# Performance work log

Hardware: AMD Instinct MI355X
Metric: run time of the kernel (lower is better)

Reference implementation:

```python
import math
import jax, jax.numpy as jnp
import numpy as np

B, S, H, NH = 2, 1536, 2048, 16
DH = H // NH  # 128
FP16_MIN = float(jnp.finfo(jnp.float16).min)


def setup_inputs() -> dict:
    key = jax.random.key(0)
    ks = jax.random.split(key, 6)
    std = 0.02
    return {
        "x": jax.random.normal(ks[0], (B, S, H), dtype=jnp.float32),
        "attention_bias": jax.random.normal(ks[1], (B, NH, S, S), dtype=jnp.float32),
        "Wq": jax.random.normal(ks[2], (H, H), dtype=jnp.float32) * std,
        "Wk": jax.random.normal(ks[3], (H, H), dtype=jnp.float32) * std,
        "Wv": jax.random.normal(ks[4], (H, H), dtype=jnp.float32) * std,
        "Wo": jax.random.normal(ks[5], (H, H), dtype=jnp.float32) * std,
    }


def reference(x, attention_bias, Wq, Wk, Wv, Wo):
    b, s, h = x.shape
    # QKV projections (nn.Linear with bias=False: y = x @ W.T)
    q = (x @ Wq.T).reshape(b, s, NH, DH).transpose(0, 2, 1, 3)  # b h s d
    k = (x @ Wk.T).reshape(b, s, NH, DH).transpose(0, 2, 1, 3)
    v = (x @ Wv.T).reshape(b, s, NH, DH).transpose(0, 2, 1, 3)
    # bias[:, :, -s:, -s:] is identity here since bias is already [b,h,s,s]
    bias = attention_bias[:, :, -s:, -s:]
    # mask where tril(bias) == 0 (upper triangle and any exact zeros in lower)
    masked = jnp.tril(bias) == 0
    bias = jnp.where(masked, FP16_MIN, bias)
    # torch SDPA default scale = 1/sqrt(head_dim) (module's softmax_scale unused)
    scale = 1.0 / math.sqrt(DH)
    scores = jnp.einsum("bhqd,bhkd->bhqk", q, k) * scale + bias
    attn = jax.nn.softmax(scores, axis=-1)
    out = jnp.einsum("bhqk,bhkd->bhqd", attn, v)  # b h s d
    out = out.transpose(0, 2, 1, 3).reshape(b, s, h)  # b s (h d)
    return out @ Wo.T
```

## Files before the change

### kernel.cpp

```cpp
#include <hip/hip_runtime.h>
#include <cstdint>
#include <stddef.h>

typedef short short8 __attribute__((ext_vector_type(8)));
typedef float floatx4 __attribute__((ext_vector_type(4)));
typedef unsigned short ushortx4 __attribute__((ext_vector_type(4)));

#define MFMA16(a, b, c) __builtin_amdgcn_mfma_f32_16x16x32_bf16((a), (b), (c), 0, 0, 0)

static constexpr int Bv = 2, Sv = 1536, Hv = 2048, NHv = 16, DHv = 128;
static constexpr int Mv = Bv * Sv;
static constexpr float SCALE = 0.08838834764831845f;

__device__ inline unsigned short f2bf(float f) {
  union { float f; unsigned u; } c; c.f = f;
  unsigned u = c.u;
  u += 0x7fffu + ((u >> 16) & 1u);
  return (unsigned short)(u >> 16);
}

__device__ inline void async_copy16(const void* g, void* l) {
  auto gp = reinterpret_cast<__attribute__((address_space(1))) uint32_t*>(
      reinterpret_cast<uintptr_t>(g));
  auto lp = reinterpret_cast<__attribute__((address_space(3))) uint32_t*>(
      reinterpret_cast<uintptr_t>(l));
  __builtin_amdgcn_global_load_lds(gp, lp, 16, 0, 0);
}

__global__ void cvt_all_kernel(const float* __restrict__ x,
    const float* __restrict__ Wq, const float* __restrict__ Wk,
    const float* __restrict__ Wv, const float* __restrict__ Wo,
    unsigned short* __restrict__ xb, unsigned short* __restrict__ wqb,
    unsigned short* __restrict__ wkb, unsigned short* __restrict__ wvb,
    unsigned short* __restrict__ wob) {
  const int i = blockIdx.x * 256 + threadIdx.x;
  const int nx4 = (Mv * Hv) / 4;
  const float* src; unsigned short* dst; int j; float scl = 1.0f;
  if (i < nx4) {
    src = x; dst = xb; j = i;
  } else {
    const int i2 = i - nx4;
    const int wsel = i2 >> 20;
    j = i2 & ((1 << 20) - 1);
    if (wsel == 0)      { src = Wq; dst = wqb; scl = SCALE; }
    else if (wsel == 1) { src = Wk; dst = wkb; }
    else if (wsel == 2) { src = Wv; dst = wvb; }
    else                { src = Wo; dst = wob; }
  }
  const float4 v = reinterpret_cast<const float4*>(src)[j];
  ushortx4 o;
  o[0] = f2bf(v.x * scl); o[1] = f2bf(v.y * scl);
  o[2] = f2bf(v.z * scl); o[3] = f2bf(v.w * scl);
  reinterpret_cast<ushortx4*>(dst)[j] = o;
}

template <int TM, bool WF32>
__global__ __launch_bounds__(256) void gemm_bt_kernel(
    const unsigned short* __restrict__ A,
    const unsigned short* __restrict__ W0, const unsigned short* __restrict__ W1,
    const unsigned short* __restrict__ W2,
    void* __restrict__ C0, void* __restrict__ C1, void* __restrict__ C2) {
  constexpr int MI = TM / 32;
  __shared__ __align__(16) unsigned short As[TM * 64];
  __shared__ __align__(16) unsigned short Bs[128 * 64];
  const int z = blockIdx.z;
  const unsigned short* W = (z == 0) ? W0 : ((z == 1) ? W1 : W2);
  const int tid = threadIdx.x;
  const int w = tid >> 6, lane = tid & 63;
  const int quad = lane >> 4, l15 = lane & 15;
  const int wr = w >> 1, wc = w & 1;
  const int tileM = blockIdx.y * TM, tileN = blockIdx.x * 128;

  floatx4 acc[MI][4];
#pragma unroll
  for (int i = 0; i < MI; ++i)
#pragma unroll
    for (int j = 0; j < 4; ++j)
#pragma unroll
      for (int r = 0; r < 4; ++r) acc[i][j][r] = 0.0f;

  size_t aoff[MI]; int alb[MI];
#pragma unroll
  for (int m = 0; m < MI; ++m) {
    const int slot = m * 256 + tid;
    const int row = slot >> 3, blk = slot & 7;
    aoff[m] = (size_t)(tileM + row) * 2048 + ((blk ^ (row & 7)) * 8);
    alb[m] = (m * 256 + w * 64) * 8;
  }
  size_t boff[4]; int blb[4];
#pragma unroll
  for (int m = 0; m < 4; ++m) {
    const int slot = m * 256 + tid;
    const int row = slot >> 3, blk = slot & 7;
    boff[m] = (size_t)(tileN + row) * 2048 + ((blk ^ (row & 7)) * 8);
    blb[m] = (m * 256 + w * 64) * 8;
  }

  for (int k0 = 0; k0 < 2048; k0 += 64) {
    __syncthreads();
#pragma unroll
    for (int m = 0; m < MI; ++m) async_copy16(A + aoff[m] + k0, As + alb[m]);
#pragma unroll
    for (int m = 0; m < 4; ++m) async_copy16(W + boff[m] + k0, Bs + blb[m]);
    __syncthreads();
#pragma unroll
    for (int kk = 0; kk < 2; ++kk) {
      const int swz = (((kk * 4 + quad) ^ (l15 & 7)) * 8);
      short8 af[MI], bfr[4];
#pragma unroll
      for (int i = 0; i < MI; ++i)
        af[i] = *(const short8*)(As + (wr * (TM / 2) + i * 16 + l15) * 64 + swz);
#pragma unroll
      for (int j = 0; j < 4; ++j)
        bfr[j] = *(const short8*)(Bs + (wc * 64 + j * 16 + l15) * 64 + swz);
#pragma unroll
      for (int i = 0; i < MI; ++i)
#pragma unroll
        for (int j = 0; j < 4; ++j) acc[i][j] = MFMA16(af[i], bfr[j], acc[i][j]);
    }
  }

  void* C = (z == 0) ? C0 : ((z == 1) ? C1 : C2);
#pragma unroll
  for (int i = 0; i < MI; ++i) {
#pragma unroll
    for (int r = 0; r < 4; ++r) {
      const int row = tileM + wr * (TM / 2) + i * 16 + quad * 4 + r;
#pragma unroll
      for (int j = 0; j < 4; ++j) {
        const int col = tileN + wc * 64 + j * 16 + l15;
        if (WF32)
          ((float*)C)[(size_t)row * 2048 + col] = acc[i][j][r];
        else
          ((unsigned short*)C)[(size_t)row * 2048 + col] = f2bf(acc[i][j][r]);
      }
    }
  }
}

__global__ __launch_bounds__(256) void vtrans_kernel(
    const unsigned short* __restrict__ V, unsigned short* __restrict__ Vtg) {
  __shared__ unsigned short Vs[64 * 132];
  const int t0 = blockIdx.x * 64, h = blockIdx.y, b = blockIdx.z;
  const int tid = threadIdx.x;
  const int w = tid >> 6, lane = tid & 63;
#pragma unroll
  for (int m = 0; m < 4; ++m) {
    const int idx = m * 256 + tid;
    const int tr = idx >> 4, blk = idx & 15;
    const unsigned short* src = V + ((size_t)(b * Sv) + t0 + tr) * Hv + h * DHv + blk * 8;
    ushortx4 v0 = *(const ushortx4*)(src);
    ushortx4 v1 = *(const ushortx4*)(src + 4);
    *(ushortx4*)(Vs + tr * 132 + blk * 8) = v0;
    *(ushortx4*)(Vs + tr * 132 + blk * 8 + 4) = v1;
  }
  __syncthreads();
  const size_t obase = ((size_t)(b * NHv + h) * DHv) * Sv + t0;
#pragma unroll 4
  for (int p = 0; p < 32; ++p) {
    const int d = p * 4 + w;
    Vtg[obase + (size_t)d * Sv + lane] = Vs[lane * 132 + d];
  }
}

__global__ __launch_bounds__(256) void attn_kernel(
    const unsigned short* __restrict__ Qg, const unsigned short* __restrict__ Kg,
    const unsigned short* __restrict__ Vtg, const float* __restrict__ bias,
    unsigned short* __restrict__ Og) {
  __shared__ __align__(16) unsigned short Ks[64 * 128];
  __shared__ __align__(16) unsigned short Vt[128 * 64];
  __shared__ __align__(16) unsigned short Ps[4 * 16 * 64];

  const int xb = blockIdx.x;
  const int qt = (xb & 1) ? (23 - (xb >> 1)) : (xb >> 1);
  const int h = blockIdx.y, b = blockIdx.z;
  const int q0 = qt * 64;
  const int tid = threadIdx.x;
  const int w = tid >> 6, lane = tid & 63;
  const int quad = lane >> 4, l15 = lane & 15;

  const size_t bh_base = (size_t)(b * Sv) * Hv + (size_t)h * DHv;
  const size_t vt_base = ((size_t)(b * NHv + h) * DHv) * Sv;

  short8 qf[4];
  {
    const unsigned short* qbase = Qg + bh_base + (size_t)(q0 + w * 16 + l15) * Hv;
#pragma unroll
    for (int kk = 0; kk < 4; ++kk)
      qf[kk] = *(const short8*)(qbase + kk * 32 + quad * 8);
  }

  floatx4 o[8];
#pragma unroll
  for (int n = 0; n < 8; ++n)
#pragma unroll
    for (int r = 0; r < 4; ++r) o[n][r] = 0.0f;
  float lrow[4] = {0.0f, 0.0f, 0.0f, 0.0f};

  const float* biasbase = bias + (size_t)(b * NHv + h) * Sv * Sv;
  unsigned short* pw = Ps + w * 1024;

  size_t koff[4], voff[4]; int lbs[4];
#pragma unroll
  for (int m = 0; m < 4; ++m) {
    const int sK = m * 256 + tid;
    const int rK = sK >> 4, bK = sK & 15;
    koff[m] = bh_base + (size_t)rK * Hv + ((bK ^ (rK & 15)) * 8);
    const int sV = m * 256 + tid;
    const int rV = sV >> 3, bV = sV & 7;
    voff[m] = vt_base + (size_t)rV * Sv + ((bV ^ (rV & 7)) * 8);
    lbs[m] = (m * 256 + w * 64) * 8;
  }

  float bv[4][4];
#pragma unroll
  for (int r = 0; r < 4; ++r) {
    const size_t brow = (size_t)(q0 + w * 16 + quad * 4 + r) * Sv;
#pragma unroll
    for (int j = 0; j < 4; ++j) bv[r][j] = biasbase[brow + j * 16 + l15];
  }

  for (int kt = 0; kt <= qt; ++kt) {
    const int k0 = kt * 64;
    __syncthreads();
#pragma unroll
    for (int m = 0; m < 4; ++m) {
      async_copy16(Kg + koff[m] + (size_t)k0 * Hv, Ks + lbs[m]);
      async_copy16(Vtg + voff[m] + k0, Vt + lbs[m]);
    }
    __syncthreads();

    const int kn = (kt < qt) ? k0 + 64 : k0;
    float bvn[4][4];
#pragma unroll
    for (int r = 0; r < 4; ++r) {
      const size_t brow = (size_t)(q0 + w * 16 + quad * 4 + r) * Sv;
#pragma unroll
      for (int j = 0; j < 4; ++j) bvn[r][j] = biasbase[brow + kn + j * 16 + l15];
    }

    floatx4 sacc[4];
#pragma unroll
    for (int j = 0; j < 4; ++j) {
#pragma unroll
      for (int r = 0; r < 4; ++r) sacc[j][r] = 0.0f;
      const int kr = j * 16 + l15;
#pragma unroll
      for (int kk = 0; kk < 4; ++kk) {
        const int g = kk * 4 + quad;
        short8 bfrag = *(const short8*)(Ks + kr * 128 + (g ^ (kr & 15)) * 8);
        sacc[j] = MFMA16(qf[kk], bfrag, sacc[j]);
      }
    }

    const bool diag = (kt == qt);
#pragma unroll
    for (int r = 0; r < 4; ++r) {
      const int qrow = q0 + w * 16 + quad * 4 + r;
      const int prow = quad * 4 + r;
      float acc_l = 0.0f;
#pragma unroll
      for (int j = 0; j < 4; ++j) {
        const int col = j * 16 + l15;
        float p = __expf(sacc[j][r] + bv[r][j]);
        if (diag && (k0 + col) > qrow) p = 0.0f;
        acc_l += p;
        pw[prow * 64 + ((col >> 3) ^ (prow & 7)) * 8 + (col & 7)] = f2bf(p);
      }
      lrow[r] += acc_l;
    }
#pragma unroll
    for (int r = 0; r < 4; ++r)
#pragma unroll
      for (int j = 0; j < 4; ++j) bv[r][j] = bvn[r][j];

#pragma unroll
    for (int kk = 0; kk < 2; ++kk) {
      const int g = kk * 4 + quad;
      short8 pa = *(const short8*)(pw + l15 * 64 + (g ^ (l15 & 7)) * 8);
#pragma unroll
      for (int n = 0; n < 8; ++n) {
        const int dr = n * 16 + l15;
        short8 vbf = *(const short8*)(Vt + dr * 64 + (g ^ (dr & 7)) * 8);
        o[n] = MFMA16(pa, vbf, o[n]);
      }
    }
  }

#pragma unroll
  for (int r = 0; r < 4; ++r) {
    float ls = lrow[r];
#pragma unroll
    for (int off = 1; off < 16; off <<= 1) ls += __shfl_xor(ls, off, 64);
    const float inv = 1.0f / ls;
    const int qrow = q0 + w * 16 + quad * 4 + r;
    const size_t rowbase = bh_base + (size_t)qrow * Hv;
#pragma unroll
    for (int n = 0; n < 8; ++n)
      Og[rowbase + n * 16 + l15] = f2bf(o[n][r] * inv);
  }
}

extern "C" void kernel_launch(void* const* d_in, const int* in_sizes, int n_in,
                              void* d_out, int out_size, void* d_ws, size_t ws_size,
                              hipStream_t stream) {
  const float* x = (const float*)d_in[0];
  const float* bias = (const float*)d_in[1];
  const float* Wq = (const float*)d_in[2];
  const float* Wk = (const float*)d_in[3];
  const float* Wv = (const float*)d_in[4];
  const float* Wo = (const float*)d_in[5];
  float* out = (float*)d_out;

  unsigned short* xb = (unsigned short*)d_ws;
  unsigned short* wqb = xb + (size_t)Mv * Hv;
  unsigned short* wkb = wqb + (size_t)Hv * Hv;
  unsigned short* wvb = wkb + (size_t)Hv * Hv;
  unsigned short* wob = wvb + (size_t)Hv * Hv;
  unsigned short* qb = wob + (size_t)Hv * Hv;
  unsigned short* kb = qb + (size_t)Mv * Hv;
  unsigned short* vb = kb + (size_t)Mv * Hv;
  unsigned short* ob = vb + (size_t)Mv * Hv;
  unsigned short* vtb = xb;
  const size_t needed = ((size_t)Mv * Hv * 5 + (size_t)Hv * Hv * 4) * 2;
  if (ws_size < needed) return;

  const int cvt_n = (Mv * Hv) / 4 + Hv * Hv;
  cvt_all_kernel<<<dim3(cvt_n / 256), 256, 0, stream>>>(
      x, Wq, Wk, Wv, Wo, xb, wqb, wkb, wvb, wob);

  gemm_bt_kernel<128, false><<<dim3(16, 24, 3), 256, 0, stream>>>(
      xb, wqb, wkb, wvb, qb, kb, vb);

  vtrans_kernel<<<dim3(24, 16, 2), 256, 0, stream>>>(vb, vtb);

  attn_kernel<<<dim3(24, NHv, Bv), 256, 0, stream>>>(qb, kb, vtb, bias, ob);

  gemm_bt_kernel<64, true><<<dim3(16, 48, 1), 256, 0, stream>>>(
      ob, wob, wob, wob, out, out, out);
}
```

Measured before the change: 628.7 us.

## Double-buffer LDS tiles in GEMM and attention kernels to overlap loads

Both the projection GEMM and the attention kernel now keep two LDS buffers per operand. Each loop iteration issues the async global-to-LDS copy for the next K/V (or A/W) tile before computing on the current one, and uses a single barrier per iteration instead of two. The aim is to hide global-load latency behind MFMA work. The cost is doubled LDS use per block, which can lower occupancy, especially in the attention kernel.

```diff
diff --git a/kernel.cpp b/kernel.cpp
--- a/kernel.cpp
+++ b/kernel.cpp
@@ -61,8 +61,8 @@
     const unsigned short* __restrict__ W2,
     void* __restrict__ C0, void* __restrict__ C1, void* __restrict__ C2) {
   constexpr int MI = TM / 32;
-  __shared__ __align__(16) unsigned short As[TM * 64];
-  __shared__ __align__(16) unsigned short Bs[128 * 64];
+  __shared__ __align__(16) unsigned short As[2][TM * 64];
+  __shared__ __align__(16) unsigned short Bs[2][128 * 64];
   const int z = blockIdx.z;
   const unsigned short* W = (z == 0) ? W0 : ((z == 1) ? W1 : W2);
   const int tid = threadIdx.x;
@@ -96,28 +96,41 @@
     blb[m] = (m * 256 + w * 64) * 8;
   }
 
-  for (int k0 = 0; k0 < 2048; k0 += 64) {
-    __syncthreads();
-#pragma unroll
-    for (int m = 0; m < MI; ++m) async_copy16(A + aoff[m] + k0, As + alb[m]);
-#pragma unroll
-    for (int m = 0; m < 4; ++m) async_copy16(W + boff[m] + k0, Bs + blb[m]);
-    __syncthreads();
+#pragma unroll
+  for (int m = 0; m < MI; ++m) async_copy16(A + aoff[m], As[0] + alb[m]);
+#pragma unroll
+  for (int m = 0; m < 4; ++m) async_copy16(W + boff[m], Bs[0] + blb[m]);
+  __syncthreads();
+
+  for (int t = 0; t < 32; ++t) {
+    const int cur = t & 1;
+    if (t < 31) {
+      const int kn = (t + 1) * 64;
+#pragma unroll
+      for (int m = 0; m < MI; ++m)
+        async_copy16(A + aoff[m] + kn, As[cur ^ 1] + alb[m]);
+#pragma unroll
+      for (int m = 0; m < 4; ++m)
+        async_copy16(W + boff[m] + kn, Bs[cur ^ 1] + blb[m]);
+    }
+    const unsigned short* as_ = As[cur];
+    const unsigned short* bs_ = Bs[cur];
 #pragma unroll
     for (int kk = 0; kk < 2; ++kk) {
       const int swz = (((kk * 4 + quad) ^ (l15 & 7)) * 8);
       short8 af[MI], bfr[4];
 #pragma unroll
       for (int i = 0; i < MI; ++i)
-        af[i] = *(const short8*)(As + (wr * (TM / 2) + i * 16 + l15) * 64 + swz);
+        af[i] = *(const short8*)(as_ + (wr * (TM / 2) + i * 16 + l15) * 64 + swz);
 #pragma unroll
       for (int j = 0; j < 4; ++j)
-        bfr[j] = *(const short8*)(Bs + (wc * 64 + j * 16 + l15) * 64 + swz);
+        bfr[j] = *(const short8*)(bs_ + (wc * 64 + j * 16 + l15) * 64 + swz);
 #pragma unroll
       for (int i = 0; i < MI; ++i)
 #pragma unroll
         for (int j = 0; j < 4; ++j) acc[i][j] = MFMA16(af[i], bfr[j], acc[i][j]);
     }
+    __syncthreads();
   }
 
   void* C = (z == 0) ? C0 : ((z == 1) ? C1 : C2);
@@ -167,8 +180,8 @@
     const unsigned short* __restrict__ Qg, const unsigned short* __restrict__ Kg,
     const unsigned short* __restrict__ Vtg, const float* __restrict__ bias,
     unsigned short* __restrict__ Og) {
-  __shared__ __align__(16) unsigned short Ks[64 * 128];
-  __shared__ __align__(16) unsigned short Vt[128 * 64];
+  __shared__ __align__(16) unsigned short Ks[2][64 * 128];
+  __shared__ __align__(16) unsigned short Vt[2][128 * 64];
   __shared__ __align__(16) unsigned short Ps[4 * 16 * 64];
 
   const int xb = blockIdx.x;
@@ -220,15 +233,25 @@
     for (int j = 0; j < 4; ++j) bv[r][j] = biasbase[brow + j * 16 + l15];
   }
 
+#pragma unroll
+  for (int m = 0; m < 4; ++m) {
+    async_copy16(Kg + koff[m], Ks[0] + lbs[m]);
+    async_copy16(Vtg + voff[m], Vt[0] + lbs[m]);
+  }
+  __syncthreads();
+
   for (int kt = 0; kt <= qt; ++kt) {
     const int k0 = kt * 64;
-    __syncthreads();
-#pragma unroll
-    for (int m = 0; m < 4; ++m) {
-      async_copy16(Kg + koff[m] + (size_t)k0 * Hv, Ks + lbs[m]);
-      async_copy16(Vtg + voff[m] + k0, Vt + lbs[m]);
-    }
-    __syncthreads();
+    const int cur = kt & 1;
+
+    if (kt < qt) {
+      const int k1 = k0 + 64;
+#pragma unroll
+      for (int m = 0; m < 4; ++m) {
+        async_copy16(Kg + koff[m] + (size_t)k1 * Hv, Ks[cur ^ 1] + lbs[m]);
+        async_copy16(Vtg + voff[m] + k1, Vt[cur ^ 1] + lbs[m]);
+      }
+    }
 
     const int kn = (kt < qt) ? k0 + 64 : k0;
     float bvn[4][4];
@@ -239,6 +262,8 @@
       for (int j = 0; j < 4; ++j) bvn[r][j] = biasbase[brow + kn + j * 16 + l15];
     }
 
+    const unsigned short* ks_ = Ks[cur];
+    const unsigned short* vt_ = Vt[cur];
     floatx4 sacc[4];
 #pragma unroll
     for (int j = 0; j < 4; ++j) {
@@ -248,7 +273,7 @@
 #pragma unroll
       for (int kk = 0; kk < 4; ++kk) {
         const int g = kk * 4 + quad;
-        short8 bfrag = *(const short8*)(Ks + kr * 128 + (g ^ (kr & 15)) * 8);
+        short8 bfrag = *(const short8*)(ks_ + kr * 128 + (g ^ (kr & 15)) * 8);
         sacc[j] = MFMA16(qf[kk], bfrag, sacc[j]);
       }
     }
@@ -281,10 +306,12 @@
 #pragma unroll
       for (int n = 0; n < 8; ++n) {
         const int dr = n * 16 + l15;
-        short8 vbf = *(const short8*)(Vt + dr * 64 + (g ^ (dr & 7)) * 8);
+        short8 vbf = *(const short8*)(vt_ + dr * 64 + (g ^ (dr & 7)) * 8);
         o[n] = MFMA16(pa, vbf, o[n]);
       }
     }
+
+    __syncthreads();
   }
 
 #pragma unroll
```

New measurement: 617.9 us. No clear change (-1.7%).
